# Performance work log

Hardware: AMD Instinct MI355X
Metric: run time of the kernel (lower is better)

Reference implementation:

```python
import jax, jax.numpy as jnp
import numpy as np

N_NODES = 500_000
N_EDGES = 1_000_000
IN_DIM = 128
HID_DIM = 256
BN_EPS = 1e-5


def setup_inputs() -> dict:
    key = jax.random.key(0)
    ks = jax.random.split(key, 4)
    out = jax.random.normal(ks[0], (N_NODES, IN_DIM), dtype=jnp.float32)
    edge_label_index = jax.random.randint(ks[1], (2, N_EDGES), 0, N_NODES, dtype=jnp.int64)
    # Kaiming-uniform-ish init scale for linears
    W1 = jax.random.normal(ks[2], (IN_DIM, HID_DIM), dtype=jnp.float32) * (1.0 / np.sqrt(IN_DIM))
    b1 = jnp.zeros((HID_DIM,), dtype=jnp.float32)
    gamma = jnp.ones((HID_DIM,), dtype=jnp.float32)
    beta = jnp.zeros((HID_DIM,), dtype=jnp.float32)
    W2 = jax.random.normal(ks[3], (HID_DIM, 1), dtype=jnp.float32) * (1.0 / np.sqrt(HID_DIM))
    b2 = jnp.zeros((1,), dtype=jnp.float32)
    return {"out": out, "edge_label_index": edge_label_index,
            "W1": W1, "b1": b1, "gamma": gamma, "beta": beta, "W2": W2, "b2": b2}


def reference(out, edge_label_index, W1, b1, gamma, beta, W2, b2):
    src = edge_label_index[0]
    dst = edge_label_index[1]
    dot = out[src] * out[dst]                      # [E, IN_DIM] gather + hadamard
    h = dot @ W1 + b1                              # [E, HID_DIM]
    # BatchNorm1d (training mode: batch statistics, biased variance)
    mean = jnp.mean(h, axis=0)
    var = jnp.mean(jnp.square(h - mean), axis=0)
    h = (h - mean) * jax.lax.rsqrt(var + BN_EPS) * gamma + beta
    h = jax.nn.relu(h)
    y = h @ W2 + b2                                # [E, 1]
    return y.reshape(-1)
```

## Files before the change

### kernel.cpp

```cpp
#include <hip/hip_runtime.h>
#include <hip/hip_bf16.h>

#define N_NODES   500000
#define E_EDGES   1000000
#define TILE_E    32
#define N_TILES   (E_EDGES / TILE_E)
#define IN_DIM_K  128
#define HID_N     256
#define BN_EPS_F  1e-5f
#define MAIN_GRID 1024
#define CONV_GRID 2048

typedef __attribute__((ext_vector_type(4))) float f32x4;
typedef __attribute__((ext_vector_type(8))) short bf16x8;

__device__ __forceinline__ unsigned short f2bf(float f) {
    __hip_bfloat16 h = __float2bfloat16(f);
    return *reinterpret_cast<unsigned short*>(&h);
}
__device__ __forceinline__ unsigned pack2(float lo, float hi) {
    return (unsigned)f2bf(lo) | ((unsigned)f2bf(hi) << 16);
}
__device__ __forceinline__ unsigned bfmul2(unsigned a, unsigned b) {
    float alo = __uint_as_float(a << 16);
    float ahi = __uint_as_float(a & 0xffff0000u);
    float blo = __uint_as_float(b << 16);
    float bhi = __uint_as_float(b & 0xffff0000u);
    return pack2(alo * blo, ahi * bhi);
}

union FragU { uint4 u; bf16x8 v; unsigned w[4]; };

__global__ void zero_stats_kernel(float* g) {
    g[threadIdx.x] = 0.0f;
}

__global__ void convert_nodes_kernel(const float* __restrict__ in,
                                     unsigned* __restrict__ out) {
    const size_t n4 = (size_t)N_NODES * IN_DIM_K / 8;
    size_t i = (size_t)blockIdx.x * blockDim.x + threadIdx.x;
    const size_t stride = (size_t)gridDim.x * blockDim.x;
    for (; i < n4; i += stride) {
        float4 a = reinterpret_cast<const float4*>(in)[2 * i];
        float4 b = reinterpret_cast<const float4*>(in)[2 * i + 1];
        uint4 o;
        o.x = pack2(a.x, a.y);
        o.y = pack2(a.z, a.w);
        o.z = pack2(b.x, b.y);
        o.w = pack2(b.z, b.w);
        reinterpret_cast<uint4*>(out)[i] = o;
    }
}

__global__ void finalize_stats_kernel(const float* __restrict__ gstat,
                                      const float* __restrict__ gamma,
                                      const float* __restrict__ beta,
                                      float* __restrict__ nAB) {
    int c = threadIdx.x;
    float inv_e = 1.0f / (float)E_EDGES;
    float mean = gstat[c] * inv_e;
    float var  = fmaxf(gstat[256 + c] * inv_e - mean * mean, 0.0f);
    float a = gamma[c] * rsqrtf(var + BN_EPS_F);
    nAB[c] = a;
    nAB[256 + c] = beta[c] - mean * a;
}

template <bool STATS, bool BFT>
__global__ __launch_bounds__(256, 2)
void hadamard_mlp_kernel(const float* __restrict__ nodes,
                         const unsigned* __restrict__ nbf,
                         const int* __restrict__ eidx,
                         const float* __restrict__ W1,
                         const float* __restrict__ W2,
                         const float* __restrict__ b2p,
                         float* __restrict__ gstat,
                         const float* __restrict__ nAB,
                         float* __restrict__ y)
{
    __shared__ unsigned sh_d[2][TILE_E * 68];
    __shared__ float s_red[2][128];

    const int tid  = threadIdx.x;
    const int lane = tid & 63;
    const int wn   = tid >> 6;
    const int l15  = lane & 15;
    const int l4   = lane >> 4;

    bf16x8 bfrag[4][4];
    #pragma unroll
    for (int nt = 0; nt < 4; ++nt) {
        const int c = wn * 64 + nt * 16 + l15;
        #pragma unroll
        for (int kk = 0; kk < 4; ++kk) {
            const int kb = kk * 32 + 8 * l4;
            FragU t;
            #pragma unroll
            for (int j = 0; j < 4; ++j) {
                float w0 = W1[(kb + 2 * j    ) * HID_N + c];
                float w1 = W1[(kb + 2 * j + 1) * HID_N + c];
                t.w[j] = pack2(w0, w1);
            }
            bfrag[nt][kk] = t.v;
        }
    }

    float a_n[4], b_n[4], w2_n[4];
    if (!STATS) {
        #pragma unroll
        for (int nt = 0; nt < 4; ++nt) {
            const int c = wn * 64 + nt * 16 + l15;
            a_n[nt]  = nAB[c];
            b_n[nt]  = nAB[256 + c];
            w2_n[nt] = W2[c];
        }
    }
    const float b2v = b2p[0];

    float s1[4] = {0.f, 0.f, 0.f, 0.f};
    float s2[4] = {0.f, 0.f, 0.f, 0.f};

    const int ge   = tid >> 3;
    const int part = tid & 7;

    uint4  gA[4], gB[4];
    float4 hA[8], hB[8];
    int siA, diA, siB, diB;

#define GATHER(GV, HV, SNODE, DNODE)                                           \
    if constexpr (BFT) {                                                       \
        const uint4* ps = reinterpret_cast<const uint4*>(nbf + (size_t)(SNODE) * 64) + part * 2; \
        const uint4* pd = reinterpret_cast<const uint4*>(nbf + (size_t)(DNODE) * 64) + part * 2; \
        GV[0] = ps[0]; GV[1] = ps[1]; GV[2] = pd[0]; GV[3] = pd[1];            \
    } else {                                                                   \
        const float4* ps = reinterpret_cast<const float4*>(nodes + (size_t)(SNODE) * IN_DIM_K) + part * 4; \
        const float4* pd = reinterpret_cast<const float4*>(nodes + (size_t)(DNODE) * IN_DIM_K) + part * 4; \
        _Pragma("unroll")                                                      \
        for (int j = 0; j < 4; ++j) { HV[j] = ps[j]; HV[4 + j] = pd[j]; }      \
    }

#define PACKBUF(GV, HV, buf)                                                   \
    if constexpr (BFT) {                                                       \
        buf[0] = bfmul2(GV[0].x, GV[2].x); buf[1] = bfmul2(GV[0].y, GV[2].y);  \
        buf[2] = bfmul2(GV[0].z, GV[2].z); buf[3] = bfmul2(GV[0].w, GV[2].w);  \
        buf[4] = bfmul2(GV[1].x, GV[3].x); buf[5] = bfmul2(GV[1].y, GV[3].y);  \
        buf[6] = bfmul2(GV[1].z, GV[3].z); buf[7] = bfmul2(GV[1].w, GV[3].w);  \
    } else {                                                                   \
        _Pragma("unroll")                                                      \
        for (int j = 0; j < 4; ++j) {                                          \
            buf[2*j]   = pack2(HV[j].x * HV[4+j].x, HV[j].y * HV[4+j].y);      \
            buf[2*j+1] = pack2(HV[j].z * HV[4+j].z, HV[j].w * HV[4+j].w);      \
        }                                                                      \
    }

    const int t0 = blockIdx.x;
    {
        const int e0 = t0 * TILE_E + ge;
        const int s = eidx[e0];
        const int d = eidx[E_EDGES + e0];
        GATHER(gA, hA, s, d);
    }
    if (t0 + MAIN_GRID < N_TILES) {
        const int e1 = (t0 + MAIN_GRID) * TILE_E + ge;
        const int s = eidx[e1];
        const int d = eidx[E_EDGES + e1];
        GATHER(gB, hB, s, d);
    }
    siA = diA = siB = diB = 0;
    if (t0 + 2 * MAIN_GRID < N_TILES) {
        const int e = (t0 + 2 * MAIN_GRID) * TILE_E + ge;
        siA = eidx[e];  diA = eidx[E_EDGES + e];
    }
    if (t0 + 3 * MAIN_GRID < N_TILES) {
        const int e = (t0 + 3 * MAIN_GRID) * TILE_E + ge;
        siB = eidx[e];  diB = eidx[E_EDGES + e];
    }

    int cur = 0;
    int ptile = -1;

#define PIPE_BODY(TILE, GV, HV, SIV, DIV)                                      \
    {                                                                          \
        const int tile_ = (TILE);                                              \
        {                       \
            unsigned buf[8];                                                   \
            PACKBUF(GV, HV, buf);                                              \
            unsigned* dst = sh_d[cur] + ge * 68 + part * 8;                    \
            *reinterpret_cast<uint4*>(dst)     = *reinterpret_cast<const uint4*>(buf);     \
            *reinterpret_cast<uint4*>(dst + 4) = *reinterpret_cast<const uint4*>(buf + 4); \
        }                                                                      \
              \
        if (tile_ + 2 * MAIN_GRID < N_TILES) {                                 \
            GATHER(GV, HV, SIV, DIV);                                          \
        }                                                                      \
                            \
        if (tile_ + 4 * MAIN_GRID < N_TILES) {                                 \
            const int e_ = (tile_ + 4 * MAIN_GRID) * TILE_E + ge;              \
            SIV = eidx[e_];  DIV = eidx[E_EDGES + e_];                         \
        }                                                                      \
        __syncthreads();                                                       \
                                     \
        if (!STATS && ptile >= 0 && tid < TILE_E) {                            \
            const float* r = s_red[cur ^ 1];                                   \
            y[ptile * TILE_E + tid] = r[tid] + r[32 + tid] + r[64 + tid]       \
                                    + r[96 + tid] + b2v;                       \
        }                                                                      \
                                  \
        f32x4 acc[2][4] = {};                                                  \
        __builtin_amdgcn_s_setprio(1);                                         \
        _Pragma("unroll")                                                      \
        for (int kk = 0; kk < 4; ++kk) {                                       \
            bf16x8 af[2];                                                      \
            _Pragma("unroll")                                                  \
            for (int mt = 0; mt < 2; ++mt) {                                   \
                const int row = mt * 16 + l15;                                 \
                FragU t;                                                       \
                t.u = *reinterpret_cast<const uint4*>(sh_d[cur] + row * 68 + kk * 16 + 4 * l4); \
                af[mt] = t.v;                                                  \
            }                                                                  \
            _Pragma("unroll")                                                  \
            for (int mt = 0; mt < 2; ++mt)                                     \
                _Pragma("unroll")                                              \
                for (int nt = 0; nt < 4; ++nt)                                 \
                    acc[mt][nt] = __builtin_amdgcn_mfma_f32_16x16x32_bf16(     \
                        af[mt], bfrag[nt][kk], acc[mt][nt], 0, 0, 0);          \
        }                                                                      \
        __builtin_amdgcn_s_setprio(0);                                         \
        if (STATS) {                                                           \
            _Pragma("unroll")                                                  \
            for (int nt = 0; nt < 4; ++nt) {                                   \
                float t1s = 0.f, t2s = 0.f;                                    \
                _Pragma("unroll")                                              \
                for (int mt = 0; mt < 2; ++mt)                                 \
                    _Pragma("unroll")                                          \
                    for (int r = 0; r < 4; ++r) {                              \
                        float v = acc[mt][nt][r];                              \
                        t1s += v;                                              \
                        t2s += v * v;                                          \
                    }                                                          \
                s1[nt] += t1s;                                                 \
                s2[nt] += t2s;                                                 \
            }                                                                  \
        } else {                                                               \
            float pw[2][4];                                                    \
            _Pragma("unroll")                                                  \
            for (int mt = 0; mt < 2; ++mt)                                     \
                _Pragma("unroll")                                              \
                for (int r = 0; r < 4; ++r) {                                  \
                    float acc_y = 0.f;                                         \
                    _Pragma("unroll")                                          \
                    for (int nt = 0; nt < 4; ++nt) {                           \
                        float z = acc[mt][nt][r] * a_n[nt] + b_n[nt];          \
                        z = fmaxf(z, 0.f);                                     \
                        acc_y += z * w2_n[nt];                                 \
                    }                                                          \
                    pw[mt][r] = acc_y;                                         \
                }                                                              \
            _Pragma("unroll")                                                  \
            for (int off = 1; off < 16; off <<= 1)                             \
                _Pragma("unroll")                                              \
                for (int mt = 0; mt < 2; ++mt)                                 \
                    _Pragma("unroll")                                          \
                    for (int r = 0; r < 4; ++r)                                \
                        pw[mt][r] += __shfl_xor(pw[mt][r], off, 64);           \
            if (l15 == 0) {                                                    \
                _Pragma("unroll")                                              \
                for (int mt = 0; mt < 2; ++mt)                                 \
                    _Pragma("unroll")                                          \
                    for (int r = 0; r < 4; ++r) {                              \
                        const int el = mt * 16 + l4 * 4 + r;                   \
                        s_red[cur][wn * 32 + el] = pw[mt][r];                  \
                    }                                                          \
            }                                                                  \
            ptile = tile_;                                                     \
        }                                                                      \
        cur ^= 1;                                                              \
    }

    for (int tile = t0; tile < N_TILES; tile += 2 * MAIN_GRID) {
        PIPE_BODY(tile, gA, hA, siA, diA);
        const int tb = tile + MAIN_GRID;
        if (tb < N_TILES) {
            PIPE_BODY(tb, gB, hB, siB, diB);
        }
    }
#undef PIPE_BODY
#undef GATHER
#undef PACKBUF

    if (STATS) {
        #pragma unroll
        for (int nt = 0; nt < 4; ++nt) {
            s1[nt] += __shfl_xor(s1[nt], 16, 64);
            s1[nt] += __shfl_xor(s1[nt], 32, 64);
            s2[nt] += __shfl_xor(s2[nt], 16, 64);
            s2[nt] += __shfl_xor(s2[nt], 32, 64);
        }
        if (l4 == 0) {
            #pragma unroll
            for (int nt = 0; nt < 4; ++nt) {
                const int c = wn * 64 + nt * 16 + l15;
                atomicAdd(&gstat[c],       s1[nt]);
                atomicAdd(&gstat[256 + c], s2[nt]);
            }
        }
    } else {
        __syncthreads();
        if (ptile >= 0 && tid < TILE_E) {
            const float* r = s_red[cur ^ 1];
            y[ptile * TILE_E + tid] = r[tid] + r[32 + tid] + r[64 + tid]
                                    + r[96 + tid] + b2v;
        }
    }
}

extern "C" void kernel_launch(void* const* d_in, const int* in_sizes, int n_in,
                              void* d_out, int out_size, void* d_ws, size_t ws_size,
                              hipStream_t stream) {
    const float* nodes = (const float*)d_in[0];
    const int*   eidx  = (const int*)d_in[1];
    const float* W1    = (const float*)d_in[2];
    const float* gamma = (const float*)d_in[4];
    const float* beta  = (const float*)d_in[5];
    const float* W2    = (const float*)d_in[6];
    const float* b2    = (const float*)d_in[7];

    float* ws    = (float*)d_ws;
    float* gstat = ws;
    float* nAB   = ws + 512;
    unsigned* nbf = (unsigned*)((char*)d_ws + 4096);
    float* y     = (float*)d_out;

    const size_t T_BYTES = (size_t)N_NODES * IN_DIM_K * 2;
    const bool fast = ws_size >= (4096 + T_BYTES);

    zero_stats_kernel<<<1, 512, 0, stream>>>(gstat);
    if (fast) {
        convert_nodes_kernel<<<CONV_GRID, 256, 0, stream>>>(nodes, nbf);
        hadamard_mlp_kernel<true, true><<<MAIN_GRID, 256, 0, stream>>>(
            nodes, nbf, eidx, W1, W2, b2, gstat, nAB, y);
        finalize_stats_kernel<<<1, 256, 0, stream>>>(gstat, gamma, beta, nAB);
        hadamard_mlp_kernel<false, true><<<MAIN_GRID, 256, 0, stream>>>(
            nodes, nbf, eidx, W1, W2, b2, gstat, nAB, y);
    } else {
        hadamard_mlp_kernel<true, false><<<MAIN_GRID, 256, 0, stream>>>(
            nodes, nbf, eidx, W1, W2, b2, gstat, nAB, y);
        finalize_stats_kernel<<<1, 256, 0, stream>>>(gstat, gamma, beta, nAB);
        hadamard_mlp_kernel<false, false><<<MAIN_GRID, 256, 0, stream>>>(
            nodes, nbf, eidx, W1, W2, b2, gstat, nAB, y);
    }
}
```

Before: 270.5 us.

## Gather FP8 node copies for the stats pass and fuse BN finalize into the kernels

The conversion kernel now also writes an FP8 copy of the node features, and the statistics pass gathers these half-size rows instead of BF16. The zero-stats and finalize kernels are folded into the convert kernel and the second MLP pass, which removes two launches. Launch bounds rise to four waves per SIMD and the second pass drops its double-buffered pipeline, both to raise occupancy. FP8 quantisation of the gathered features makes the batch-norm mean and variance less accurate, and each block of the second pass recomputes the normalisation constants.

```diff
diff --git a/kernel.cpp b/kernel.cpp
--- a/kernel.cpp
+++ b/kernel.cpp
@@ -8,10 +8,12 @@
 #define IN_DIM_K  128
 #define HID_N     256
 #define BN_EPS_F  1e-5f
-#define MAIN_GRID 1024
+#define FAST_GRID 1024
+#define FB_GRID   768
 #define CONV_GRID 2048
 
 typedef __attribute__((ext_vector_type(4))) float f32x4;
+typedef __attribute__((ext_vector_type(2))) float f32x2;
 typedef __attribute__((ext_vector_type(8))) short bf16x8;
 
 __device__ __forceinline__ unsigned short f2bf(float f) {
@@ -28,6 +30,20 @@
     float bhi = __uint_as_float(b & 0xffff0000u);
     return pack2(alo * blo, ahi * bhi);
 }
+__device__ __forceinline__ void fp8mul4(unsigned ws, unsigned wd,
+                                        unsigned& lo, unsigned& hi) {
+    f32x2 s01 = __builtin_amdgcn_cvt_pk_f32_fp8(ws, false);
+    f32x2 s23 = __builtin_amdgcn_cvt_pk_f32_fp8(ws, true);
+    f32x2 d01 = __builtin_amdgcn_cvt_pk_f32_fp8(wd, false);
+    f32x2 d23 = __builtin_amdgcn_cvt_pk_f32_fp8(wd, true);
+    lo = pack2(s01[0] * d01[0], s01[1] * d01[1]);
+    hi = pack2(s23[0] * d23[0], s23[1] * d23[1]);
+}
+__device__ __forceinline__ unsigned pk8(float4 a) {
+    int r = __builtin_amdgcn_cvt_pk_fp8_f32(a.x, a.y, 0, false);
+    r = __builtin_amdgcn_cvt_pk_fp8_f32(a.z, a.w, r, true);
+    return (unsigned)r;
+}
 
 union FragU { uint4 u; bf16x8 v; unsigned w[4]; };
 
@@ -35,8 +51,15 @@
     g[threadIdx.x] = 0.0f;
 }
 
+template <bool F8>
 __global__ void convert_nodes_kernel(const float* __restrict__ in,
-                                     unsigned* __restrict__ out) {
+                                     unsigned* __restrict__ out16,
+                                     unsigned* __restrict__ out8,
+                                     float* __restrict__ gstat) {
+    if (blockIdx.x == 0) {
+        gstat[threadIdx.x] = 0.0f;
+        gstat[256 + threadIdx.x] = 0.0f;
+    }
     const size_t n4 = (size_t)N_NODES * IN_DIM_K / 8;
     size_t i = (size_t)blockIdx.x * blockDim.x + threadIdx.x;
     const size_t stride = (size_t)gridDim.x * blockDim.x;
@@ -48,33 +71,28 @@
         o.y = pack2(a.z, a.w);
         o.z = pack2(b.x, b.y);
         o.w = pack2(b.z, b.w);
-        reinterpret_cast<uint4*>(out)[i] = o;
-    }
-}
-
-__global__ void finalize_stats_kernel(const float* __restrict__ gstat,
-                                      const float* __restrict__ gamma,
-                                      const float* __restrict__ beta,
-                                      float* __restrict__ nAB) {
-    int c = threadIdx.x;
-    float inv_e = 1.0f / (float)E_EDGES;
-    float mean = gstat[c] * inv_e;
-    float var  = fmaxf(gstat[256 + c] * inv_e - mean * mean, 0.0f);
-    float a = gamma[c] * rsqrtf(var + BN_EPS_F);
-    nAB[c] = a;
-    nAB[256 + c] = beta[c] - mean * a;
-}
-
-template <bool STATS, bool BFT>
-__global__ __launch_bounds__(256, 2)
+        reinterpret_cast<uint4*>(out16)[i] = o;
+        if (F8) {
+            uint2 p;
+            p.x = pk8(a);
+            p.y = pk8(b);
+            reinterpret_cast<uint2*>(out8)[i] = p;
+        }
+    }
+}
+
+template <bool STATS, int MODE, bool D2, int MINW>
+__global__ __launch_bounds__(256, MINW)
 void hadamard_mlp_kernel(const float* __restrict__ nodes,
                          const unsigned* __restrict__ nbf,
+                         const unsigned* __restrict__ nf8,
                          const int* __restrict__ eidx,
                          const float* __restrict__ W1,
                          const float* __restrict__ W2,
                          const float* __restrict__ b2p,
                          float* __restrict__ gstat,
-                         const float* __restrict__ nAB,
+                         const float* __restrict__ gamma,
+                         const float* __restrict__ beta,
                          float* __restrict__ y)
 {
     __shared__ unsigned sh_d[2][TILE_E * 68];
@@ -106,11 +124,17 @@
 
     float a_n[4], b_n[4], w2_n[4];
     if (!STATS) {
+        const float inv_e = 1.0f / (float)E_EDGES;
         #pragma unroll
         for (int nt = 0; nt < 4; ++nt) {
             const int c = wn * 64 + nt * 16 + l15;
-            a_n[nt]  = nAB[c];
-            b_n[nt]  = nAB[256 + c];
+            float s  = gstat[c];
+            float ss = gstat[256 + c];
+            float mean = s * inv_e;
+            float var  = fmaxf(ss * inv_e - mean * mean, 0.0f);
+            float a = gamma[c] * rsqrtf(var + BN_EPS_F);
+            a_n[nt]  = a;
+            b_n[nt]  = beta[c] - mean * a;
             w2_n[nt] = W2[c];
         }
     }
@@ -122,12 +146,18 @@
     const int ge   = tid >> 3;
     const int part = tid & 7;
 
-    uint4  gA[4], gB[4];
-    float4 hA[8], hB[8];
+    const int G = gridDim.x;
+    const int NEXT_OFF = (D2 ? 2 : 1) * G;
+
+    uint4  ga[4], gb[4];
+    float4 ha[8], hb[8];
     int siA, diA, siB, diB;
 
 #define GATHER(GV, HV, SNODE, DNODE)                                           \
-    if constexpr (BFT) {                                                       \
+    if constexpr (MODE == 2) {                                                 \
+        GV[0] = *(reinterpret_cast<const uint4*>(nf8 + (size_t)(SNODE) * 32) + part); \
+        GV[1] = *(reinterpret_cast<const uint4*>(nf8 + (size_t)(DNODE) * 32) + part); \
+    } else if constexpr (MODE == 1) {                                          \
         const uint4* ps = reinterpret_cast<const uint4*>(nbf + (size_t)(SNODE) * 64) + part * 2; \
         const uint4* pd = reinterpret_cast<const uint4*>(nbf + (size_t)(DNODE) * 64) + part * 2; \
         GV[0] = ps[0]; GV[1] = ps[1]; GV[2] = pd[0]; GV[3] = pd[1];            \
@@ -138,40 +168,26 @@
         for (int j = 0; j < 4; ++j) { HV[j] = ps[j]; HV[4 + j] = pd[j]; }      \
     }
 
-#define PACKBUF(GV, HV, buf)                                                   \
-    if constexpr (BFT) {                                                       \
-        buf[0] = bfmul2(GV[0].x, GV[2].x); buf[1] = bfmul2(GV[0].y, GV[2].y);  \
-        buf[2] = bfmul2(GV[0].z, GV[2].z); buf[3] = bfmul2(GV[0].w, GV[2].w);  \
-        buf[4] = bfmul2(GV[1].x, GV[3].x); buf[5] = bfmul2(GV[1].y, GV[3].y);  \
-        buf[6] = bfmul2(GV[1].z, GV[3].z); buf[7] = bfmul2(GV[1].w, GV[3].w);  \
-    } else {                                                                   \
-        _Pragma("unroll")                                                      \
-        for (int j = 0; j < 4; ++j) {                                          \
-            buf[2*j]   = pack2(HV[j].x * HV[4+j].x, HV[j].y * HV[4+j].y);      \
-            buf[2*j+1] = pack2(HV[j].z * HV[4+j].z, HV[j].w * HV[4+j].w);      \
-        }                                                                      \
-    }
-
     const int t0 = blockIdx.x;
     {
         const int e0 = t0 * TILE_E + ge;
         const int s = eidx[e0];
         const int d = eidx[E_EDGES + e0];
-        GATHER(gA, hA, s, d);
-    }
-    if (t0 + MAIN_GRID < N_TILES) {
-        const int e1 = (t0 + MAIN_GRID) * TILE_E + ge;
+        GATHER(ga, ha, s, d);
+    }
+    if (D2 && t0 + G < N_TILES) {
+        const int e1 = (t0 + G) * TILE_E + ge;
         const int s = eidx[e1];
         const int d = eidx[E_EDGES + e1];
-        GATHER(gB, hB, s, d);
+        GATHER(gb, hb, s, d);
     }
     siA = diA = siB = diB = 0;
-    if (t0 + 2 * MAIN_GRID < N_TILES) {
-        const int e = (t0 + 2 * MAIN_GRID) * TILE_E + ge;
+    if (t0 + NEXT_OFF < N_TILES) {
+        const int e = (t0 + NEXT_OFF) * TILE_E + ge;
         siA = eidx[e];  diA = eidx[E_EDGES + e];
     }
-    if (t0 + 3 * MAIN_GRID < N_TILES) {
-        const int e = (t0 + 3 * MAIN_GRID) * TILE_E + ge;
+    if (D2 && t0 + G + NEXT_OFF < N_TILES) {
+        const int e = (t0 + G + NEXT_OFF) * TILE_E + ge;
         siB = eidx[e];  diB = eidx[E_EDGES + e];
     }
 
@@ -181,30 +197,44 @@
 #define PIPE_BODY(TILE, GV, HV, SIV, DIV)                                      \
     {                                                                          \
         const int tile_ = (TILE);                                              \
-        {                       \
+        {          \
             unsigned buf[8];                                                   \
-            PACKBUF(GV, HV, buf);                                              \
+            if constexpr (MODE == 2) {                                         \
+                fp8mul4(GV[0].x, GV[1].x, buf[0], buf[1]);                     \
+                fp8mul4(GV[0].y, GV[1].y, buf[2], buf[3]);                     \
+                fp8mul4(GV[0].z, GV[1].z, buf[4], buf[5]);                     \
+                fp8mul4(GV[0].w, GV[1].w, buf[6], buf[7]);                     \
+            } else if constexpr (MODE == 1) {                                  \
+                buf[0] = bfmul2(GV[0].x, GV[2].x); buf[1] = bfmul2(GV[0].y, GV[2].y); \
+                buf[2] = bfmul2(GV[0].z, GV[2].z); buf[3] = bfmul2(GV[0].w, GV[2].w); \
+                buf[4] = bfmul2(GV[1].x, GV[3].x); buf[5] = bfmul2(GV[1].y, GV[3].y); \
+                buf[6] = bfmul2(GV[1].z, GV[3].z); buf[7] = bfmul2(GV[1].w, GV[3].w); \
+            } else {                                                           \
+                _Pragma("unroll")                                              \
+                for (int j = 0; j < 4; ++j) {                                  \
+                    buf[2*j]   = pack2(HV[j].x * HV[4+j].x, HV[j].y * HV[4+j].y); \
+                    buf[2*j+1] = pack2(HV[j].z * HV[4+j].z, HV[j].w * HV[4+j].w); \
+                }                                                              \
+            }                                                                  \
             unsigned* dst = sh_d[cur] + ge * 68 + part * 8;                    \
             *reinterpret_cast<uint4*>(dst)     = *reinterpret_cast<const uint4*>(buf);     \
             *reinterpret_cast<uint4*>(dst + 4) = *reinterpret_cast<const uint4*>(buf + 4); \
         }                                                                      \
-              \
-        if (tile_ + 2 * MAIN_GRID < N_TILES) {                                 \
+                          \
+        if (tile_ + NEXT_OFF < N_TILES) {                                      \
             GATHER(GV, HV, SIV, DIV);                                          \
         }                                                                      \
-                            \
-        if (tile_ + 4 * MAIN_GRID < N_TILES) {                                 \
-            const int e_ = (tile_ + 4 * MAIN_GRID) * TILE_E + ge;              \
+                                        \
+        if (tile_ + 2 * NEXT_OFF < N_TILES) {                                  \
+            const int e_ = (tile_ + 2 * NEXT_OFF) * TILE_E + ge;               \
             SIV = eidx[e_];  DIV = eidx[E_EDGES + e_];                         \
         }                                                                      \
         __syncthreads();                                                       \
-                                     \
         if (!STATS && ptile >= 0 && tid < TILE_E) {                            \
             const float* r = s_red[cur ^ 1];                                   \
             y[ptile * TILE_E + tid] = r[tid] + r[32 + tid] + r[64 + tid]       \
                                     + r[96 + tid] + b2v;                       \
         }                                                                      \
-                                  \
         f32x4 acc[2][4] = {};                                                  \
         __builtin_amdgcn_s_setprio(1);                                         \
         _Pragma("unroll")                                                      \
@@ -276,16 +306,21 @@
         cur ^= 1;                                                              \
     }
 
-    for (int tile = t0; tile < N_TILES; tile += 2 * MAIN_GRID) {
-        PIPE_BODY(tile, gA, hA, siA, diA);
-        const int tb = tile + MAIN_GRID;
-        if (tb < N_TILES) {
-            PIPE_BODY(tb, gB, hB, siB, diB);
+    if constexpr (!D2) {
+        for (int tile = t0; tile < N_TILES; tile += G) {
+            PIPE_BODY(tile, ga, ha, siA, diA);
+        }
+    } else {
+        for (int tile = t0; tile < N_TILES; tile += 2 * G) {
+            PIPE_BODY(tile, ga, ha, siA, diA);
+            const int tb = tile + G;
+            if (tb < N_TILES) {
+                PIPE_BODY(tb, gb, hb, siB, diB);
+            }
         }
     }
 #undef PIPE_BODY
 #undef GATHER
-#undef PACKBUF
 
     if (STATS) {
         #pragma unroll
@@ -326,26 +361,32 @@
 
     float* ws    = (float*)d_ws;
     float* gstat = ws;
-    float* nAB   = ws + 512;
+    const size_t BF_BYTES = (size_t)N_NODES * IN_DIM_K * 2;
+    const size_t F8_BYTES = (size_t)N_NODES * IN_DIM_K;
     unsigned* nbf = (unsigned*)((char*)d_ws + 4096);
+    unsigned* nf8 = (unsigned*)((char*)d_ws + 4096 + BF_BYTES);
     float* y     = (float*)d_out;
 
-    const size_t T_BYTES = (size_t)N_NODES * IN_DIM_K * 2;
-    const bool fast = ws_size >= (4096 + T_BYTES);
-
-    zero_stats_kernel<<<1, 512, 0, stream>>>(gstat);
-    if (fast) {
-        convert_nodes_kernel<<<CONV_GRID, 256, 0, stream>>>(nodes, nbf);
-        hadamard_mlp_kernel<true, true><<<MAIN_GRID, 256, 0, stream>>>(
-            nodes, nbf, eidx, W1, W2, b2, gstat, nAB, y);
-        finalize_stats_kernel<<<1, 256, 0, stream>>>(gstat, gamma, beta, nAB);
-        hadamard_mlp_kernel<false, true><<<MAIN_GRID, 256, 0, stream>>>(
-            nodes, nbf, eidx, W1, W2, b2, gstat, nAB, y);
+    const bool lvl2 = ws_size >= 4096 + BF_BYTES + F8_BYTES;
+    const bool lvl1 = ws_size >= 4096 + BF_BYTES;
+
+    if (lvl2) {
+        convert_nodes_kernel<true><<<CONV_GRID, 256, 0, stream>>>(nodes, nbf, nf8, gstat);
+        hadamard_mlp_kernel<true, 2, true, 4><<<FAST_GRID, 256, 0, stream>>>(
+            nodes, nbf, nf8, eidx, W1, W2, b2, gstat, gamma, beta, y);
+        hadamard_mlp_kernel<false, 1, false, 4><<<FAST_GRID, 256, 0, stream>>>(
+            nodes, nbf, nf8, eidx, W1, W2, b2, gstat, gamma, beta, y);
+    } else if (lvl1) {
+        convert_nodes_kernel<false><<<CONV_GRID, 256, 0, stream>>>(nodes, nbf, nf8, gstat);
+        hadamard_mlp_kernel<true, 1, false, 4><<<FAST_GRID, 256, 0, stream>>>(
+            nodes, nbf, nf8, eidx, W1, W2, b2, gstat, gamma, beta, y);
+        hadamard_mlp_kernel<false, 1, false, 4><<<FAST_GRID, 256, 0, stream>>>(
+            nodes, nbf, nf8, eidx, W1, W2, b2, gstat, gamma, beta, y);
     } else {
-        hadamard_mlp_kernel<true, false><<<MAIN_GRID, 256, 0, stream>>>(
-            nodes, nbf, eidx, W1, W2, b2, gstat, nAB, y);
-        finalize_stats_kernel<<<1, 256, 0, stream>>>(gstat, gamma, beta, nAB);
-        hadamard_mlp_kernel<false, false><<<MAIN_GRID, 256, 0, stream>>>(
-            nodes, nbf, eidx, W1, W2, b2, gstat, nAB, y);
-    }
-}
+        zero_stats_kernel<<<1, 512, 0, stream>>>(gstat);
+        hadamard_mlp_kernel<true, 0, false, 3><<<FB_GRID, 256, 0, stream>>>(
+            nodes, nbf, nf8, eidx, W1, W2, b2, gstat, gamma, beta, y);
+        hadamard_mlp_kernel<false, 0, false, 3><<<FB_GRID, 256, 0, stream>>>(
+            nodes, nbf, nf8, eidx, W1, W2, b2, gstat, gamma, beta, y);
+    }
+}
```

New measurement: 462.0 us. 70.8% more time.
